# Kernel optimization log

Hardware: AMD Instinct MI355X
Metric: run time of the kernel (lower is better)

Reference implementation:

```python
import jax, jax.numpy as jnp
import numpy as np
from jax import lax
from jax.scipy.special import erf

EPS = 1e-5
B = 256

def _conv(x, w, stride):
    return lax.conv_general_dilated(x, w, (stride, stride), ((1, 1), (1, 1)),
                                    dimension_numbers=('NCHW', 'OIHW', 'NCHW'))

def lr_conv(x, alpha, betta, bias, stride):
    # Ternary weight distribution (LR-nets): p0 = P(w=0), p1 = P(w=1)
    p0 = jax.nn.sigmoid(alpha)
    p1 = (1.0 - p0) * jax.nn.sigmoid(betta)
    w_mean = 2.0 * p1 + p0 - 1.0          # E[w] = p1 - p_{-1}
    w_var = (1.0 - p0) - w_mean * w_mean  # Var[w] = E[w^2] - E[w]^2
    m = _conv(x, w_mean, stride) + bias[None, :, None, None]
    v = _conv(x * x, w_var, stride)
    return m, v

def sign_prob(m, v):
    # expected sign under CLT Gaussian: 2*Phi(m/sqrt(v)) - 1 = erf(m / sqrt(2 v))
    return erf(m / jnp.sqrt(2.0 * (v + EPS)))

def setup_inputs() -> dict:
    key = jax.random.key(0)
    ks = jax.random.split(key, 32)
    def n(k, shape, s=1.0):
        return jax.random.normal(k, shape, dtype=jnp.float32) * s
    inp = {}
    inp['x'] = n(ks[0], (B, 3, 32, 32))
    shapes = [(128, 3), (128, 128), (256, 128), (256, 256), (512, 256), (512, 512)]
    i = 1
    for li, (co, ci) in enumerate(shapes, start=1):
        inp['a%d' % li] = n(ks[i], (co, ci, 3, 3)); i += 1
        inp['b%d' % li] = n(ks[i], (co, ci, 3, 3)); i += 1
        inp['c%d' % li] = jnp.zeros((co,), jnp.float32)
    inp['bn_gamma'] = jnp.ones((512,), jnp.float32)
    inp['bn_beta'] = jnp.zeros((512,), jnp.float32)
    inp['fc1_w'] = n(ks[20], (1024, 8192), 0.01)
    inp['fc1_b'] = jnp.zeros((1024,), jnp.float32)
    inp['fc2_w'] = n(ks[21], (10, 1024), 0.03)
    inp['fc2_b'] = jnp.zeros((10,), jnp.float32)
    inp['noise6'] = n(ks[22], (B, 512, 4, 4))
    return inp

def reference(x, a1, b1, c1, a2, b2, c2, a3, b3, c3, a4, b4, c4, a5, b5, c5,
              a6, b6, c6, bn_gamma, bn_beta, fc1_w, fc1_b, fc2_w, fc2_b, noise6):
    h = x
    for (a, bt, c, s) in [(a1, b1, c1, 1), (a2, b2, c2, 2), (a3, b3, c3, 1),
                          (a4, b4, c4, 2), (a5, b5, c5, 1)]:
        m, v = lr_conv(h, a, bt, c, s)
        h = sign_prob(m, v)
    m, v = lr_conv(h, a6, b6, c6, 2)          # output_sample=True layer
    z = m + jnp.sqrt(v + EPS) * noise6        # reparameterized Gaussian sample
    mu = jnp.mean(z, axis=(0, 2, 3), keepdims=True)
    var = jnp.var(z, axis=(0, 2, 3), keepdims=True)
    z = bn_gamma[None, :, None, None] * (z - mu) / jnp.sqrt(var + EPS) + bn_beta[None, :, None, None]
    z = jax.nn.relu(z).reshape(z.shape[0], -1)  # [B, 8192]
    z = jax.nn.relu(z @ fc1_w.T + fc1_b)
    return z @ fc2_w.T + fc2_b
```

## Files before the change

### kernel.cpp

```cpp
#include <hip/hip_runtime.h>
#include <hip/hip_bf16.h>
#include <math.h>

#define EPS 1e-5f

typedef __hip_bfloat16 bf16;
typedef short s16x8 __attribute__((ext_vector_type(8)));
typedef float f32x4 __attribute__((ext_vector_type(4)));

constexpr int ilog2c(int v) { return v <= 1 ? 0 : 1 + ilog2c(v >> 1); }

__device__ __forceinline__ float ldin(const void* p, size_t i, int isbf) {
    return isbf ? __bfloat162float(((const bf16*)p)[i]) : ((const float*)p)[i];
}
__device__ __forceinline__ float b2f_bits(short s) {
    unsigned u = ((unsigned)(unsigned short)s) << 16;
    return __builtin_bit_cast(float, u);
}
__device__ __forceinline__ unsigned sqpk1(unsigned w) {
    float lo = __builtin_bit_cast(float, w << 16);
    float hi = __builtin_bit_cast(float, w & 0xffff0000u);
    lo *= lo; hi *= hi;
    unsigned ul = __builtin_bit_cast(unsigned, lo) + 0x8000u;
    unsigned uh = __builtin_bit_cast(unsigned, hi) + 0x8000u;
    return __builtin_amdgcn_perm(uh, ul, 0x07060302);
}
__device__ __forceinline__ uint4 sqpk4(uint4 u) {
    uint4 r;
    r.x = sqpk1(u.x); r.y = sqpk1(u.y); r.z = sqpk1(u.z); r.w = sqpk1(u.w);
    return r;
}

__device__ __forceinline__ void dma16(const void* g, void* l) {
    __builtin_amdgcn_global_load_lds(
        (const __attribute__((address_space(1))) void*)g,
        (__attribute__((address_space(3))) void*)l, 16, 0, 0);
}

__global__ __launch_bounds__(64) void detect_kernel(const void* __restrict__ x,
                                                    int* __restrict__ flags,
                                                    char* __restrict__ gA,
                                                    char* __restrict__ gB) {
    const unsigned* w = (const unsigned*)x;
    unsigned word = w[threadIdx.x];
    int e = (word >> 23) & 0xFF;
    bool ok = (word == 0u) || (e >= 0x70 && e <= 0x8E);
    unsigned long long m = __ballot(ok);
    if (threadIdx.x == 0) flags[0] = (__popcll(m) >= 32) ? 0 : 1;
    if (threadIdx.x < 16) ((uint4*)gA)[threadIdx.x] = (uint4){0, 0, 0, 0};
    else if (threadIdx.x < 32) ((uint4*)gB)[threadIdx.x - 16] = (uint4){0, 0, 0, 0};
}

__global__ __launch_bounds__(256) void prep_w_l1(
    const void* __restrict__ alpha, const void* __restrict__ betta,
    const int* __restrict__ flags, float* __restrict__ wmv, int n)
{
    int i = blockIdx.x * 256 + threadIdx.x;
    if (i >= n) return;
    int fl = flags[0];
    float a = ldin(alpha, i, fl), b = ldin(betta, i, fl);
    float p0 = 1.f / (1.f + expf(-a));
    float p1 = (1.f - p0) / (1.f + expf(-b));
    float m = 2.f * p1 + p0 - 1.f;
    wmv[i] = m;
    wmv[n + i] = (1.f - p0) - m * m;
}

__global__ __launch_bounds__(256) void prep_w_r(
    const void* __restrict__ alpha, const void* __restrict__ betta,
    const int* __restrict__ flags, bf16* __restrict__ wmr, bf16* __restrict__ wvr,
    int lc, int n)
{
    int o = blockIdx.x * 256 + threadIdx.x;
    if (o >= n) return;
    int fl = flags[0];
    int cotap = o >> lc;
    int ci = o & ((1 << lc) - 1);
    int co = cotap / 9;
    int tap = cotap - co * 9;
    int i = (((co << lc) + ci) * 9) + tap;
    float a = ldin(alpha, i, fl), b = ldin(betta, i, fl);
    float p0 = 1.f / (1.f + expf(-a));
    float p1 = (1.f - p0) / (1.f + expf(-b));
    float m = 2.f * p1 + p0 - 1.f;
    float v = (1.f - p0) - m * m;
    wmr[o] = __float2bfloat16(m);
    wvr[o] = __float2bfloat16(v);
}

__global__ __launch_bounds__(256) void permute_fc1(
    const void* __restrict__ w, const int* __restrict__ flags, bf16* __restrict__ wp)
{
    __shared__ float L[8192];
    const int fl = flags[0];
    int tid = threadIdx.x;
    int o = blockIdx.x;
    size_t srow = (size_t)o * 8192;
    for (int c = tid; c < 512; c += 256) {
        float v[16];
        if (fl) {
            const uint4* s = (const uint4*)((const bf16*)w + srow + c * 16);
            uint4 u0 = s[0], u1 = s[1];
            const unsigned short* h0 = (const unsigned short*)&u0;
            const unsigned short* h1 = (const unsigned short*)&u1;
#pragma unroll
            for (int j = 0; j < 8; j++) { v[j] = b2f_bits((short)h0[j]); v[8 + j] = b2f_bits((short)h1[j]); }
        } else {
            const float4* s = (const float4*)((const float*)w + srow + c * 16);
#pragma unroll
            for (int j = 0; j < 4; j++) {
                float4 t4 = s[j];
                v[j * 4 + 0] = t4.x; v[j * 4 + 1] = t4.y; v[j * 4 + 2] = t4.z; v[j * 4 + 3] = t4.w;
            }
        }
#pragma unroll
        for (int hw = 0; hw < 16; hw++) L[hw * 512 + c] = v[hw];
    }
    __syncthreads();
    for (int j = 0; j < 32; j++) {
        int idx = j * 256 + tid;
        wp[srow + idx] = __float2bfloat16(L[idx]);
    }
}

__global__ __launch_bounds__(256) void l1_conv(
    const void* __restrict__ x, const float* __restrict__ wmv,
    const void* __restrict__ bias, const int* __restrict__ flags,
    bf16* __restrict__ out)
{
    __shared__ float Xs[64][28];
    const int fl = flags[0];
    int tid = threadIdx.x;
    int pos0 = blockIdx.x * 64;
    int b = pos0 >> 10;
    for (int u = tid; u < 576; u += 256) {
        int p = u / 9, r = u - p * 9;
        int ci = r / 3, kh = r - ci * 3;
        int pos = pos0 + p;
        int oh = (pos >> 5) & 31, ow = pos & 31;
        int ih = oh - 1 + kh;
        bool okh = (unsigned)ih < 32u;
        size_t base = ((size_t)(b * 3 + ci) * 32 + ih) * 32;
#pragma unroll
        for (int kw = 0; kw < 3; kw++) {
            int iw = ow - 1 + kw;
            float v = (okh && (unsigned)iw < 32u) ? ldin(x, base + iw, fl) : 0.f;
            Xs[p][ci * 9 + kh * 3 + kw] = v;
        }
    }
    int c = tid & 127, pg = tid >> 7;
    float wm[27], wv[27];
#pragma unroll
    for (int k = 0; k < 27; k++) {
        wm[k] = wmv[c * 27 + k];
        wv[k] = wmv[3456 + c * 27 + k];
    }
    float bs = ldin(bias, c, fl);
    __syncthreads();
    for (int it = 0; it < 32; it++) {
        int p = it * 2 + pg;
        float aM = 0.f, aV = 0.f;
#pragma unroll
        for (int k = 0; k < 27; k++) {
            float xv = Xs[p][k];
            aM = fmaf(xv, wm[k], aM);
            aV = fmaf(xv * xv, wv[k], aV);
        }
        out[(size_t)(pos0 + p) * 128 + c] =
            __float2bfloat16(erff((aM + bs) * rsqrtf(2.f * (aV + EPS))));
    }
}

template<int CI, int CO, int H, int W, int S, int OH, int OW, int ACT, int COT>
__global__ __launch_bounds__(256, 4) void conv_gemm(
    const char* __restrict__ xreg,
    int zpoff,
    const bf16* __restrict__ wmr,
    const bf16* __restrict__ wvr,
    const void* __restrict__ bias, const void* __restrict__ noise,
    const int* __restrict__ flags, void* __restrict__ outp)
{
    constexpr int OHW = OH * OW;
    constexpr int KC = CI / 32;
    constexpr int NC = 9 * KC;
    constexpr int WJ = COT / 32;
    constexpr int NW = COT / 16;
    constexpr int XB = 128 * 64;
    constexpr int WB = COT * 64;
    constexpr int BUFB = XB + 2 * WB;
    constexpr int LOHW = ilog2c(OHW), LOW = ilog2c(OW);
    static_assert((NC & 1) == 0 && COT == 64, "");

    __shared__ __align__(16) char smem[2 * BUFB];

    const int tid = threadIdx.x;
    const int lane = tid & 63, wv_ = tid >> 6;
    const int q = lane >> 4, l15 = lane & 15;
    const int pw = (wv_ >> 1) * 64, cw = (wv_ & 1) * (16 * WJ);
    const int c0 = blockIdx.y * COT;
    const int bx128 = blockIdx.x * 128;

    const int sl   = (lane & 7) ^ (lane >> 3);
    const int row2 = 2 * (lane >> 3) + (sl >> 2);
    const int u16b = (sl & 3) * 16;

    int xb[4], ohS[4], owS[4];
#pragma unroll
    for (int kk = 0; kk < 4; kk++) {
        int P = bx128 + 16 * ((wv_ & 1) * 4 + kk) + row2;
        int bi = P >> LOHW;
        ohS[kk] = ((P >> LOW) & (OH - 1)) * S - 1;
        owS[kk] = (P & (OW - 1)) * S - 1;
        xb[kk] = bi * (H * W * CI * 2);
    }
    const char* wsb = (const char*)((wv_ == 3) ? wvr : wmr)
                      + (size_t)(c0 + row2) * (9 * CI * 2) + u16b;
    const int wdoff = XB + ((wv_ == 3) ? WB : 0);

    const int lA = (l15 >> 1) * 128 + (((((l15 & 1) << 2) | q) ^ (l15 >> 1)) << 4);
    const int abase = pw * 64 + lA;
    const int bbase = cw * 64 + lA;

    f32x4 accM[4][WJ], accV[4][WJ];
#pragma unroll
    for (int i = 0; i < 4; i++)
#pragma unroll
        for (int j = 0; j < WJ; j++) {
            accM[i][j] = (f32x4){0.f, 0.f, 0.f, 0.f};
            accV[i][j] = (f32x4){0.f, 0.f, 0.f, 0.f};
        }

    auto stage = [&](int t, int nb) {
        char* buf = smem + nb * BUFB;
        if (wv_ < 2) {
            const int tap = t / KC, kci = (t - tap * KC) * 64;
            const int kh = tap / 3, kw2 = tap - 3 * kh;
#pragma unroll
            for (int kk = 0; kk < 4; kk++) {
                int ih = ohS[kk] + kh, iw = owS[kk] + kw2;
                bool ok = ((unsigned)ih < (unsigned)H) && ((unsigned)iw < (unsigned)W);
                int off = xb[kk] + (ih * W + iw) * (CI * 2) + kci + u16b;
                off = ok ? off : zpoff;
                dma16(xreg + off, buf + ((wv_ & 1) * 4 + kk) * 1024);
            }
        } else {
            const char* s = wsb + t * 64;
            char* d = buf + wdoff;
#pragma unroll
            for (int k = 0; k < NW; k++)
                dma16(s + (size_t)k * (16 * 9 * CI * 2), d + k * 1024);
        }
    };

    auto compute = [&](int nb) {
        const char* buf = smem + nb * BUFB;
        s16x8 bm[WJ], bv[WJ];
#pragma unroll
        for (int j = 0; j < WJ; j++) {
            bm[j] = *(const s16x8*)(buf + XB + bbase + j * 1024);
            bv[j] = *(const s16x8*)(buf + XB + WB + bbase + j * 1024);
        }
#pragma unroll
        for (int i = 0; i < 4; i++) {
            s16x8 a = *(const s16x8*)(buf + abase + i * 1024);
            uint4 uq = sqpk4(*(const uint4*)&a);
            s16x8 aq = *(const s16x8*)&uq;
#pragma unroll
            for (int j = 0; j < WJ; j++) {
                accM[i][j] = __builtin_amdgcn_mfma_f32_16x16x32_bf16(a,  bm[j], accM[i][j], 0, 0, 0);
                accV[i][j] = __builtin_amdgcn_mfma_f32_16x16x32_bf16(aq, bv[j], accV[i][j], 0, 0, 0);
            }
        }
    };

#define BAR() asm volatile("s_waitcnt vmcnt(0) lgkmcnt(0)\n\ts_barrier" ::: "memory")

    stage(0, 0);
    for (int t = 0; t < NC; t += 2) {
        BAR();
        if (t + 1 < NC) stage(t + 1, 1);
        compute(0);
        BAR();
        if (t + 2 < NC) stage(t + 2, 0);
        compute(1);
    }
#undef BAR

    __syncthreads();
    const int fl = flags[0];
    if constexpr (ACT == 0) {
        bf16* Lact = (bf16*)smem;
        constexpr int LCB = ilog2c(COT * 2);
#pragma unroll
        for (int j = 0; j < WJ; j++) {
            int co = c0 + cw + j * 16 + l15;
            float bs = ldin(bias, co, fl);
#pragma unroll
            for (int i = 0; i < 4; i++) {
#pragma unroll
                for (int r = 0; r < 4; r++) {
                    int PPl = pw + i * 16 + q * 4 + r;
                    float mm = accM[i][j][r] + bs, vv = accV[i][j][r];
                    Lact[PPl * COT + cw + j * 16 + l15] =
                        __float2bfloat16(erff(mm * rsqrtf(2.f * (vv + EPS))));
                }
            }
        }
        __syncthreads();
        constexpr int NST = (128 * COT * 2) / 4096;
#pragma unroll
        for (int k = 0; k < NST; k++) {
            int f = k * 4096 + tid * 16;
            int rowl = f >> LCB;
            int colb = f & ((COT * 2) - 1);
            uint4 va = *(const uint4*)((char*)smem + f);
            size_t gb = ((size_t)(bx128 + rowl) * CO + c0) * 2 + colb;
            *(uint4*)((char*)outp + gb) = va;
        }
    } else {
#pragma unroll
        for (int j = 0; j < WJ; j++) {
            int co = c0 + cw + j * 16 + l15;
            float bs = ldin(bias, co, fl);
#pragma unroll
            for (int i = 0; i < 4; i++) {
#pragma unroll
                for (int r = 0; r < 4; r++) {
                    int PP = bx128 + pw + i * 16 + q * 4 + r;
                    float mm = accM[i][j][r] + bs, vv = accV[i][j][r];
                    int bb = PP / OHW, hw = PP % OHW;
                    float nz = ldin(noise, ((size_t)bb * CO + co) * OHW + hw, fl);
                    ((float*)outp)[(size_t)PP * CO + co] = mm + sqrtf(vv + EPS) * nz;
                }
            }
        }
    }
}

__global__ __launch_bounds__(256) void fc1_gemm_sk(
    const bf16* __restrict__ A, const bf16* __restrict__ Wp,
    float* __restrict__ part)
{
    __shared__ bf16 Xs[128 * 40];
    __shared__ bf16 Ws[128 * 40];
    int tid = threadIdx.x;
    int lane = tid & 63, wv_ = tid >> 6;
    int q = lane >> 4, l15 = lane & 15;
    const int pw = (wv_ >> 1) * 64, cw = (wv_ & 1) * 64;
    const int p0 = blockIdx.x * 128, c0 = blockIdx.y * 128;
    const int kb = blockIdx.z * 1024;
    const int row_i = tid >> 1, half = tid & 1;

    f32x4 acc[4][4];
#pragma unroll
    for (int i = 0; i < 4; i++)
#pragma unroll
        for (int j = 0; j < 4; j++) acc[i][j] = (f32x4){0.f, 0.f, 0.f, 0.f};

    for (int k0 = kb; k0 < kb + 1024; k0 += 32) {
        __syncthreads();
        {
            const uint4* s = (const uint4*)(A + (size_t)(p0 + row_i) * 8192 + k0 + half * 16);
            uint4* d = (uint4*)(Xs + row_i * 40 + half * 16);
            d[0] = s[0]; d[1] = s[1];
        }
        {
            const uint4* s = (const uint4*)(Wp + (size_t)(c0 + row_i) * 8192 + k0 + half * 16);
            uint4* d = (uint4*)(Ws + row_i * 40 + half * 16);
            d[0] = s[0]; d[1] = s[1];
        }
        __syncthreads();
        s16x8 a[4], bb[4];
#pragma unroll
        for (int i = 0; i < 4; i++) {
            a[i]  = *(const s16x8*)(Xs + (pw + i * 16 + l15) * 40 + q * 8);
            bb[i] = *(const s16x8*)(Ws + (cw + i * 16 + l15) * 40 + q * 8);
        }
#pragma unroll
        for (int i = 0; i < 4; i++)
#pragma unroll
            for (int j = 0; j < 4; j++)
                acc[i][j] = __builtin_amdgcn_mfma_f32_16x16x32_bf16(a[i], bb[j], acc[i][j], 0, 0, 0);
    }

    float* pbase = part + (size_t)blockIdx.z * 256 * 1024;
#pragma unroll
    for (int j = 0; j < 4; j++) {
        int co = c0 + cw + j * 16 + l15;
#pragma unroll
        for (int i = 0; i < 4; i++) {
            f32x4 m4 = acc[i][j];
#pragma unroll
            for (int r = 0; r < 4; r++) {
                int P = p0 + pw + i * 16 + q * 4 + r;
                pbase[(size_t)P * 1024 + co] = m4[r];
            }
        }
    }
}

__global__ __launch_bounds__(256) void fc1_reduce(
    const float* __restrict__ part, const void* __restrict__ bias,
    const int* __restrict__ flags, float* __restrict__ out)
{
    int i = blockIdx.x * 256 + threadIdx.x;
    float s = 0.f;
#pragma unroll
    for (int k = 0; k < 8; k++) s += part[(size_t)k * 262144 + i];
    out[i] = fmaxf(s + ldin(bias, i & 1023, flags[0]), 0.f);
}

__global__ __launch_bounds__(256) void bn_part(const float* __restrict__ z,
                                               float4* __restrict__ partial)
{
    int blk = blockIdx.x;
    int t = threadIdx.x;
    float s0 = 0, ss0 = 0, s1 = 0, ss1 = 0;
    for (int p = 0; p < 32; p++) {
        float2 v = ((const float2*)z)[((size_t)(blk * 32 + p)) * 256 + t];
        s0 += v.x; ss0 += v.x * v.x;
        s1 += v.y; ss1 += v.y * v.y;
    }
    partial[blk * 256 + t] = make_float4(s0, ss0, s1, ss1);
}

__global__ __launch_bounds__(512) void bn_fin(
    const float4* __restrict__ partial, const void* __restrict__ gamma,
    const void* __restrict__ beta, const int* __restrict__ flags,
    float* __restrict__ sc, float* __restrict__ sh)
{
    int c = threadIdx.x;
    float s = 0, ss = 0;
    for (int j = 0; j < 128; j++) {
        float4 pv = partial[j * 256 + (c >> 1)];
        s += (c & 1) ? pv.z : pv.x;
        ss += (c & 1) ? pv.w : pv.y;
    }
    float mean = s * (1.f / 4096.f);
    float var = ss * (1.f / 4096.f) - mean * mean;
    int fl = flags[0];
    float scale = ldin(gamma, c, fl) * rsqrtf(var + EPS);
    sc[c] = scale;
    sh[c] = ldin(beta, c, fl) - mean * scale;
}

__global__ __launch_bounds__(256) void bn_apply(
    const float* __restrict__ z, const float* __restrict__ sc,
    const float* __restrict__ sh, bf16* __restrict__ zr)
{
    int i = blockIdx.x * 256 + threadIdx.x;
    int c = i & 511;
    float v = z[i] * sc[c] + sh[c];
    zr[i] = __float2bfloat16(fmaxf(v, 0.f));
}

__global__ __launch_bounds__(640) void fc2_kernel(
    const float* __restrict__ A, const void* __restrict__ W,
    const void* __restrict__ bias, const int* __restrict__ flags,
    void* __restrict__ out)
{
    const int fl = flags[0];
    int n = blockIdx.x;
    int o = threadIdx.x >> 6;
    int lane = threadIdx.x & 63;
    const float* a = A + (size_t)n * 1024;
    size_t wbase = (size_t)o * 1024;
    float s = 0.f;
    for (int i = lane; i < 1024; i += 64) s = fmaf(a[i], ldin(W, wbase + i, fl), s);
#pragma unroll
    for (int off = 32; off > 0; off >>= 1) s += __shfl_down(s, off);
    if (lane == 0) {
        float v = s + ldin(bias, o, fl);
        if (fl) ((bf16*)out)[n * 10 + o] = __float2bfloat16(v);
        else    ((float*)out)[n * 10 + o] = v;
    }
}

extern "C" void kernel_launch(void* const* d_in, const int* in_sizes, int n_in,
                              void* d_out, int out_size, void* d_ws, size_t ws_size,
                              hipStream_t stream)
{
    const void* x = d_in[0];
    const void *al[6], *be[6], *bi[6];
    for (int l = 0; l < 6; l++) {
        al[l] = d_in[1 + 3 * l];
        be[l] = d_in[2 + 3 * l];
        bi[l] = d_in[3 + 3 * l];
    }
    const void* bn_gamma = d_in[19];
    const void* bn_beta  = d_in[20];
    const void* fc1_w = d_in[21];
    const void* fc1_b = d_in[22];
    const void* fc2_w = d_in[23];
    const void* fc2_b = d_in[24];
    const void* noise = d_in[25];

    char* base = (char*)d_ws;
    size_t off = 0;
    auto alloc = [&](size_t bytes) { void* p = base + off; off += (bytes + 255) & ~(size_t)255; return p; };
    int* flags = (int*)alloc(256);
    float* w1 = (float*)alloc(2 * 3456 * sizeof(float));
    const int SwLC[5] = {7, 7, 8, 8, 9};
    const size_t Sw[5] = {147456, 294912, 589824, 1179648, 2359296};
    bf16 *wmr[5], *wvr[5];
    for (int l = 0; l < 5; l++) {
        wmr[l] = (bf16*)alloc(Sw[l] * sizeof(bf16));
        wvr[l] = (bf16*)alloc(Sw[l] * sizeof(bf16));
    }
    bf16* Wp   = (bf16*)alloc((size_t)1024 * 8192 * sizeof(bf16));
    float4* part = (float4*)alloc((size_t)128 * 256 * sizeof(float4));
    float* bnsc = (float*)alloc(512 * sizeof(float));
    float* bnsh = (float*)alloc(512 * sizeof(float));
    float* fc1o = (float*)alloc((size_t)256 * 1024 * sizeof(float));
    bf16* zr   = (bf16*)alloc((size_t)256 * 8192 * sizeof(bf16));

    const int ZPA = 67108864;
    const int ZPB = 16777216;
    char* RA = (char*)alloc((size_t)ZPA + 256);
    char* RB = (char*)alloc((size_t)ZPB + 256);
    float* z = (float*)RB;
    float* fc1part = (float*)(RB + 8388608);

    detect_kernel<<<1, 64, 0, stream>>>(x, flags, RA + ZPA, RB + ZPB);

    prep_w_l1<<<14, 256, 0, stream>>>(al[0], be[0], flags, w1, 3456);
    for (int l = 0; l < 5; l++) {
        int n = (int)Sw[l];
        prep_w_r<<<(n + 255) / 256, 256, 0, stream>>>(
            al[l + 1], be[l + 1], flags, wmr[l], wvr[l], SwLC[l], n);
    }
    permute_fc1<<<1024, 256, 0, stream>>>(fc1_w, flags, Wp);

    l1_conv<<<4096, 256, 0, stream>>>(x, w1, bi[0], flags, (bf16*)RA);

    conv_gemm<128, 128, 32, 32, 2, 16, 16, 0, 64><<<dim3(512, 2), 256, 0, stream>>>(
        RA, ZPA, wmr[0], wvr[0], bi[1], nullptr, flags, RB);
    conv_gemm<128, 256, 16, 16, 1, 16, 16, 0, 64><<<dim3(512, 4), 256, 0, stream>>>(
        RB, ZPB, wmr[1], wvr[1], bi[2], nullptr, flags, RA);
    conv_gemm<256, 256, 16, 16, 2, 8, 8, 0, 64><<<dim3(128, 4), 256, 0, stream>>>(
        RA, ZPA, wmr[2], wvr[2], bi[3], nullptr, flags, RB);
    conv_gemm<256, 512, 8, 8, 1, 8, 8, 0, 64><<<dim3(128, 8), 256, 0, stream>>>(
        RB, ZPB, wmr[3], wvr[3], bi[4], nullptr, flags, RA);
    conv_gemm<512, 512, 8, 8, 2, 4, 4, 1, 64><<<dim3(32, 8), 256, 0, stream>>>(
        RA, ZPA, wmr[4], wvr[4], bi[5], noise, flags, z);

    bn_part<<<128, 256, 0, stream>>>(z, part);
    bn_fin<<<1, 512, 0, stream>>>(part, bn_gamma, bn_beta, flags, bnsc, bnsh);
    bn_apply<<<8192, 256, 0, stream>>>(z, bnsc, bnsh, zr);

    fc1_gemm_sk<<<dim3(2, 8, 8), 256, 0, stream>>>(zr, Wp, fc1part);
    fc1_reduce<<<1024, 256, 0, stream>>>(fc1part, fc1_b, flags, fc1o);
    fc2_kernel<<<256, 640, 0, stream>>>(fc1o, fc2_w, fc2_b, flags, d_out);
}
```

Before: 764.0 us.

## Precompute squared activations in conv epilogue and double fc1 split-K

```diff
diff --git a/kernel.cpp b/kernel.cpp
--- a/kernel.cpp
+++ b/kernel.cpp
@@ -171,14 +171,15 @@
     }
 }
 
-template<int CI, int CO, int H, int W, int S, int OH, int OW, int ACT, int COT>
-__global__ __launch_bounds__(256, 4) void conv_gemm(
+template<int CI, int CO, int H, int W, int S, int OH, int OW, int ACT, int SQX, int COT>
+__global__ __launch_bounds__(256, 3) void conv_gemm(
     const char* __restrict__ xreg,
-    int zpoff,
+    int sqoff, int zpoff,
     const bf16* __restrict__ wmr,
     const bf16* __restrict__ wvr,
     const void* __restrict__ bias, const void* __restrict__ noise,
-    const int* __restrict__ flags, void* __restrict__ outp)
+    const int* __restrict__ flags,
+    void* __restrict__ outp, bf16* __restrict__ outsq)
 {
     constexpr int OHW = OH * OW;
     constexpr int KC = CI / 32;
@@ -187,7 +188,7 @@
     constexpr int NW = COT / 16;
     constexpr int XB = 128 * 64;
     constexpr int WB = COT * 64;
-    constexpr int BUFB = XB + 2 * WB;
+    constexpr int BUFB = 2 * XB + 2 * WB;
     constexpr int LOHW = ilog2c(OHW), LOW = ilog2c(OW);
     static_assert((NC & 1) == 0 && COT == 64, "");
 
@@ -204,18 +205,19 @@
     const int row2 = 2 * (lane >> 3) + (sl >> 2);
     const int u16b = (sl & 3) * 16;
 
-    int xb[4], ohS[4], owS[4];
-#pragma unroll
-    for (int kk = 0; kk < 4; kk++) {
-        int P = bx128 + 16 * ((wv_ & 1) * 4 + kk) + row2;
+    int xb[8], ohS[8], owS[8];
+#pragma unroll
+    for (int kk = 0; kk < 8; kk++) {
+        int P = bx128 + 16 * kk + row2;
         int bi = P >> LOHW;
         ohS[kk] = ((P >> LOW) & (OH - 1)) * S - 1;
         owS[kk] = (P & (OW - 1)) * S - 1;
-        xb[kk] = bi * (H * W * CI * 2);
+        xb[kk] = bi * (H * W * CI * 2) + ((!SQX && wv_ == 1) ? sqoff : 0);
     }
     const char* wsb = (const char*)((wv_ == 3) ? wvr : wmr)
                       + (size_t)(c0 + row2) * (9 * CI * 2) + u16b;
-    const int wdoff = XB + ((wv_ == 3) ? WB : 0);
+    const int wdoff = 2 * XB + ((wv_ == 3) ? WB : 0);
+    const int xdoff = (wv_ == 1) ? XB : 0;
 
     const int lA = (l15 >> 1) * 128 + (((((l15 & 1) << 2) | q) ^ (l15 >> 1)) << 4);
     const int abase = pw * 64 + lA;
@@ -230,25 +232,46 @@
             accV[i][j] = (f32x4){0.f, 0.f, 0.f, 0.f};
         }
 
-    auto stage = [&](int t, int nb) {
-        char* buf = smem + nb * BUFB;
-        if (wv_ < 2) {
-            const int tap = t / KC, kci = (t - tap * KC) * 64;
-            const int kh = tap / 3, kw2 = tap - 3 * kh;
-#pragma unroll
-            for (int kk = 0; kk < 4; kk++) {
-                int ih = ohS[kk] + kh, iw = owS[kk] + kw2;
-                bool ok = ((unsigned)ih < (unsigned)H) && ((unsigned)iw < (unsigned)W);
-                int off = xb[kk] + (ih * W + iw) * (CI * 2) + kci + u16b;
-                off = ok ? off : zpoff;
-                dma16(xreg + off, buf + ((wv_ & 1) * 4 + kk) * 1024);
-            }
-        } else {
-            const char* s = wsb + t * 64;
-            char* d = buf + wdoff;
-#pragma unroll
-            for (int k = 0; k < NW; k++)
-                dma16(s + (size_t)k * (16 * 9 * CI * 2), d + k * 1024);
+    uint4 g[4];
+
+    auto stageX = [&](int t, char* buf) {
+        const int tap = t / KC, kci = (t - tap * KC) * 64;
+        const int kh = tap / 3, kw2 = tap - 3 * kh;
+#pragma unroll
+        for (int kk = 0; kk < 8; kk++) {
+            int ih = ohS[kk] + kh, iw = owS[kk] + kw2;
+            bool ok = ((unsigned)ih < (unsigned)H) && ((unsigned)iw < (unsigned)W);
+            int off = xb[kk] + (ih * W + iw) * (CI * 2) + kci + u16b;
+            off = ok ? off : zpoff;
+            dma16(xreg + off, buf + xdoff + kk * 1024);
+        }
+    };
+    auto stageW = [&](int t, char* buf) {
+        const char* s = wsb + t * 64;
+        char* d = buf + wdoff;
+#pragma unroll
+        for (int k = 0; k < NW; k++)
+            dma16(s + (size_t)k * (16 * 9 * CI * 2), d + k * 1024);
+    };
+    auto loadX = [&](int t) {
+        const int tap = t / KC, kci = (t - tap * KC) * 64;
+        const int kh = tap / 3, kw2 = tap - 3 * kh;
+#pragma unroll
+        for (int ts = 0; ts < 4; ts++) {
+            const int kk = (wv_ & 1) * 4 + ts;
+            int ih = ohS[kk] + kh, iw = owS[kk] + kw2;
+            bool ok = ((unsigned)ih < (unsigned)H) && ((unsigned)iw < (unsigned)W);
+            int off = xb[kk] + (ih * W + iw) * (CI * 2) + kci + u16b;
+            g[ts] = (uint4){0, 0, 0, 0};
+            if (ok) g[ts] = *(const uint4*)(xreg + off);
+        }
+    };
+    auto writeX = [&](char* buf) {
+#pragma unroll
+        for (int ts = 0; ts < 4; ts++) {
+            const int kk = (wv_ & 1) * 4 + ts;
+            *(uint4*)(buf + kk * 1024 + lane * 16) = g[ts];
+            *(uint4*)(buf + XB + kk * 1024 + lane * 16) = sqpk4(g[ts]);
         }
     };
 
@@ -257,14 +280,13 @@
         s16x8 bm[WJ], bv[WJ];
 #pragma unroll
         for (int j = 0; j < WJ; j++) {
-            bm[j] = *(const s16x8*)(buf + XB + bbase + j * 1024);
-            bv[j] = *(const s16x8*)(buf + XB + WB + bbase + j * 1024);
+            bm[j] = *(const s16x8*)(buf + 2 * XB + bbase + j * 1024);
+            bv[j] = *(const s16x8*)(buf + 2 * XB + WB + bbase + j * 1024);
         }
 #pragma unroll
         for (int i = 0; i < 4; i++) {
-            s16x8 a = *(const s16x8*)(buf + abase + i * 1024);
-            uint4 uq = sqpk4(*(const uint4*)&a);
-            s16x8 aq = *(const s16x8*)&uq;
+            s16x8 a  = *(const s16x8*)(buf + abase + i * 1024);
+            s16x8 aq = *(const s16x8*)(buf + XB + abase + i * 1024);
 #pragma unroll
             for (int j = 0; j < WJ; j++) {
                 accM[i][j] = __builtin_amdgcn_mfma_f32_16x16x32_bf16(a,  bm[j], accM[i][j], 0, 0, 0);
@@ -275,22 +297,37 @@
 
 #define BAR() asm volatile("s_waitcnt vmcnt(0) lgkmcnt(0)\n\ts_barrier" ::: "memory")
 
-    stage(0, 0);
+    if (wv_ >= 2) stageW(0, smem);
+    else if constexpr (!SQX) stageX(0, smem);
+    else { loadX(0); writeX(smem); }
+    BAR();
+
     for (int t = 0; t < NC; t += 2) {
+        if constexpr (!SQX) {
+            if (t + 1 < NC) { if (wv_ < 2) stageX(t + 1, smem + BUFB); else stageW(t + 1, smem + BUFB); }
+            compute(0);
+        } else {
+            if (t + 1 < NC) { if (wv_ >= 2) stageW(t + 1, smem + BUFB); else loadX(t + 1); }
+            compute(0);
+            if (t + 1 < NC && wv_ < 2) writeX(smem + BUFB);
+        }
         BAR();
-        if (t + 1 < NC) stage(t + 1, 1);
-        compute(0);
+        if constexpr (!SQX) {
+            if (t + 2 < NC) { if (wv_ < 2) stageX(t + 2, smem); else stageW(t + 2, smem); }
+            compute(1);
+        } else {
+            if (t + 2 < NC) { if (wv_ >= 2) stageW(t + 2, smem); else loadX(t + 2); }
+            compute(1);
+            if (t + 2 < NC && wv_ < 2) writeX(smem);
+        }
         BAR();
-        if (t + 2 < NC) stage(t + 2, 0);
-        compute(1);
     }
 #undef BAR
 
-    __syncthreads();
     const int fl = flags[0];
     if constexpr (ACT == 0) {
         bf16* Lact = (bf16*)smem;
-        constexpr int LCB = ilog2c(COT * 2);
+        bf16* Lsq  = (bf16*)(smem + 128 * COT * 2);
 #pragma unroll
         for (int j = 0; j < WJ; j++) {
             int co = c0 + cw + j * 16 + l15;
@@ -301,21 +338,28 @@
                 for (int r = 0; r < 4; r++) {
                     int PPl = pw + i * 16 + q * 4 + r;
                     float mm = accM[i][j][r] + bs, vv = accV[i][j][r];
-                    Lact[PPl * COT + cw + j * 16 + l15] =
-                        __float2bfloat16(erff(mm * rsqrtf(2.f * (vv + EPS))));
+                    float y = erff(mm * rsqrtf(2.f * (vv + EPS)));
+                    bf16 yb = __float2bfloat16(y);
+                    float yf = __bfloat162float(yb);
+                    int lc = cw + j * 16 + l15;
+                    Lact[PPl * COT + lc] = yb;
+                    Lsq [PPl * COT + lc] = __float2bfloat16(yf * yf);
                 }
             }
         }
         __syncthreads();
+        constexpr int LCB = ilog2c(COT * 2);
         constexpr int NST = (128 * COT * 2) / 4096;
 #pragma unroll
         for (int k = 0; k < NST; k++) {
             int f = k * 4096 + tid * 16;
             int rowl = f >> LCB;
             int colb = f & ((COT * 2) - 1);
-            uint4 va = *(const uint4*)((char*)smem + f);
+            uint4 va = *(const uint4*)((char*)Lact + f);
+            uint4 vs = *(const uint4*)((char*)Lsq + f);
             size_t gb = ((size_t)(bx128 + rowl) * CO + c0) * 2 + colb;
             *(uint4*)((char*)outp + gb) = va;
+            *(uint4*)((char*)outsq + gb) = vs;
         }
     } else {
 #pragma unroll
@@ -348,7 +392,7 @@
     int q = lane >> 4, l15 = lane & 15;
     const int pw = (wv_ >> 1) * 64, cw = (wv_ & 1) * 64;
     const int p0 = blockIdx.x * 128, c0 = blockIdx.y * 128;
-    const int kb = blockIdx.z * 1024;
+    const int kb = blockIdx.z * 512;
     const int row_i = tid >> 1, half = tid & 1;
 
     f32x4 acc[4][4];
@@ -357,7 +401,7 @@
 #pragma unroll
         for (int j = 0; j < 4; j++) acc[i][j] = (f32x4){0.f, 0.f, 0.f, 0.f};
 
-    for (int k0 = kb; k0 < kb + 1024; k0 += 32) {
+    for (int k0 = kb; k0 < kb + 512; k0 += 32) {
         __syncthreads();
         {
             const uint4* s = (const uint4*)(A + (size_t)(p0 + row_i) * 8192 + k0 + half * 16);
@@ -406,7 +450,7 @@
     int i = blockIdx.x * 256 + threadIdx.x;
     float s = 0.f;
 #pragma unroll
-    for (int k = 0; k < 8; k++) s += part[(size_t)k * 262144 + i];
+    for (int k = 0; k < 16; k++) s += part[(size_t)k * 262144 + i];
     out[i] = fmaxf(s + ldin(bias, i & 1023, flags[0]), 0.f);
 }
 
@@ -515,7 +559,7 @@
     bf16* zr   = (bf16*)alloc((size_t)256 * 8192 * sizeof(bf16));
 
     const int ZPA = 67108864;
-    const int ZPB = 16777216;
+    const int ZPB = 33554432;
     char* RA = (char*)alloc((size_t)ZPA + 256);
     char* RB = (char*)alloc((size_t)ZPB + 256);
     float* z = (float*)RB;
@@ -533,22 +577,27 @@
 
     l1_conv<<<4096, 256, 0, stream>>>(x, w1, bi[0], flags, (bf16*)RA);
 
-    conv_gemm<128, 128, 32, 32, 2, 16, 16, 0, 64><<<dim3(512, 2), 256, 0, stream>>>(
-        RA, ZPA, wmr[0], wvr[0], bi[1], nullptr, flags, RB);
-    conv_gemm<128, 256, 16, 16, 1, 16, 16, 0, 64><<<dim3(512, 4), 256, 0, stream>>>(
-        RB, ZPB, wmr[1], wvr[1], bi[2], nullptr, flags, RA);
-    conv_gemm<256, 256, 16, 16, 2, 8, 8, 0, 64><<<dim3(128, 4), 256, 0, stream>>>(
-        RA, ZPA, wmr[2], wvr[2], bi[3], nullptr, flags, RB);
-    conv_gemm<256, 512, 8, 8, 1, 8, 8, 0, 64><<<dim3(128, 8), 256, 0, stream>>>(
-        RB, ZPB, wmr[3], wvr[3], bi[4], nullptr, flags, RA);
-    conv_gemm<512, 512, 8, 8, 2, 4, 4, 1, 64><<<dim3(32, 8), 256, 0, stream>>>(
-        RA, ZPA, wmr[4], wvr[4], bi[5], noise, flags, z);
+    conv_gemm<128, 128, 32, 32, 2, 16, 16, 0, 1, 64><<<dim3(512, 2), 256, 0, stream>>>(
+        RA, 0, ZPA, wmr[0], wvr[0], bi[1], nullptr, flags,
+        RB, (bf16*)(RB + 16777216));
+    conv_gemm<128, 256, 16, 16, 1, 16, 16, 0, 0, 64><<<dim3(512, 4), 256, 0, stream>>>(
+        RB, 16777216, ZPB, wmr[1], wvr[1], bi[2], nullptr, flags,
+        RA, (bf16*)(RA + 33554432));
+    conv_gemm<256, 256, 16, 16, 2, 8, 8, 0, 0, 64><<<dim3(128, 4), 256, 0, stream>>>(
+        RA, 33554432, ZPA, wmr[2], wvr[2], bi[3], nullptr, flags,
+        RB, (bf16*)(RB + 8388608));
+    conv_gemm<256, 512, 8, 8, 1, 8, 8, 0, 0, 64><<<dim3(128, 8), 256, 0, stream>>>(
+        RB, 8388608, ZPB, wmr[3], wvr[3], bi[4], nullptr, flags,
+        RA, (bf16*)(RA + 16777216));
+    conv_gemm<512, 512, 8, 8, 2, 4, 4, 1, 0, 64><<<dim3(32, 8), 256, 0, stream>>>(
+        RA, 16777216, ZPA, wmr[4], wvr[4], bi[5], noise, flags,
+        z, nullptr);
 
     bn_part<<<128, 256, 0, stream>>>(z, part);
     bn_fin<<<1, 512, 0, stream>>>(part, bn_gamma, bn_beta, flags, bnsc, bnsh);
     bn_apply<<<8192, 256, 0, stream>>>(z, bnsc, bnsh, zr);
 
-    fc1_gemm_sk<<<dim3(2, 8, 8), 256, 0, stream>>>(zr, Wp, fc1part);
+    fc1_gemm_sk<<<dim3(2, 8, 16), 256, 0, stream>>>(zr, Wp, fc1part);
     fc1_reduce<<<1024, 256, 0, stream>>>(fc1part, fc1_b, flags, fc1o);
     fc2_kernel<<<256, 640, 0, stream>>>(fc1o, fc2_w, fc2_b, flags, d_out);
 }
```

Result: slower. 814.2 us (+6.6%).
